# Kernel optimization log

Measured on AMD Instinct MI355X. Metric: run time of the kernel, lower is better.

## Reference

```python
import jax, jax.numpy as jnp
import numpy as np

TOKENS = 8192
IN_FEATURES = 4096
OUT_FEATURES = 4096
ALPHA = 2e-05
BETA = 8.0


def setup_inputs() -> dict:
    key = jax.random.key(0)
    kx, kw = jax.random.split(key)
    # int8 activations and weights, values in [-127, 127]
    x = jax.random.randint(kx, (TOKENS, IN_FEATURES), -127, 128, dtype=jnp.int32).astype(jnp.int8)
    weight = jax.random.randint(kw, (OUT_FEATURES, IN_FEATURES), -127, 128, dtype=jnp.int32).astype(jnp.int8)
    bias = jnp.zeros((OUT_FEATURES,), dtype=jnp.float32)
    a = jnp.float32(ALPHA)  # dequant scale: input_scale * weight_scale
    b = jnp.float32(BETA)   # requant scale: 1 / out_scale
    return {"x": x, "weight": weight, "bias": bias, "a": a, "b": b}


def reference(x, weight, bias, a, b):
    acc = jnp.matmul(x.astype(jnp.int32), weight.T.astype(jnp.int32))
    # fp32 epilogue: dequant scale + bias, exact GeLU, requant by beta
    y = a * acc.astype(jnp.float32) + bias[None, :]
    y = jax.nn.gelu(y, approximate=False)
    # quantize output to int8 (round to nearest even, saturate)
    q = jnp.clip(jnp.rint(y * b), -128.0, 127.0).astype(jnp.int8)
    return q
```

## Files before the change

### kernel.cpp

```cpp
#include <hip/hip_runtime.h>
#include <cstdint>
#include <cstddef>

#define TOKENS 8192
#define INF    4096
#define OUTF   4096

typedef int v4i __attribute__((ext_vector_type(4)));

__global__ __launch_bounds__(256) void pack_i8_kernel(
    const int* __restrict__ xi, const int* __restrict__ wi,
    uint8_t* __restrict__ x8, uint8_t* __restrict__ w8) {
  const int NX = (TOKENS * INF) / 4;
  const int NT = 2048 * 256;
  int tid = blockIdx.x * 256 + threadIdx.x;
#pragma unroll 1
  for (int g = 0; g < 6; ++g) {
    int c[4];
    int4 v[4];
#pragma unroll
    for (int j = 0; j < 4; ++j) {
      c[j] = (g * 4 + j) * NT + tid;
      const int4* src = (c[j] < NX) ? ((const int4*)xi + c[j])
                                    : ((const int4*)wi + (c[j] - NX));
      v[j] = *src;
    }
#pragma unroll
    for (int j = 0; j < 4; ++j) {
      unsigned* dst = (c[j] < NX) ? ((unsigned*)x8 + c[j])
                                  : ((unsigned*)w8 + (c[j] - NX));
      *dst = (v[j].x & 255) | ((v[j].y & 255) << 8) | ((v[j].z & 255) << 16) |
             (((unsigned)v[j].w) << 24);
    }
  }
}

__device__ __forceinline__ float gelu_exact(float y) {
  float x = y * 0.70710678118654752f;
  float s = fabsf(x);
  float t = __builtin_amdgcn_rcpf(fmaf(s, 0.3275911f, 1.0f));
  float p = t * fmaf(t, fmaf(t, fmaf(t, fmaf(t, 1.061405429f, -1.453152027f),
                                     1.421413741f), -0.284496736f),
                     0.254829592f);
  float e = __expf(-s * s);
  float er = fmaf(-p, e, 1.0f);
  er = copysignf(er, x);
  return 0.5f * y * (1.0f + er);
}

__device__ __forceinline__ void barrier_fenced() {
  asm volatile("" ::: "memory");
  __builtin_amdgcn_s_barrier();
  asm volatile("" ::: "memory");
}

__global__ __launch_bounds__(512, 2) void gemm_i8_gelu_q_kernel(
    const uint8_t* __restrict__ x8, const uint8_t* __restrict__ w8,
    const float* __restrict__ bias, const float* __restrict__ pa,
    const float* __restrict__ pb, int* __restrict__ out) {
  __shared__ char sm[131072];

  const int tid = threadIdx.x;
  const int l   = tid & 63;
  const int wv  = tid >> 6;
  const int wr  = wv >> 2;
  const int wc  = wv & 3;
  const int lr  = l & 15;
  const int lg  = l >> 4;

  int id = blockIdx.x;
  int wg = (id & 7) * 64 + (id >> 3);
  const int m0 = (wg >> 4) * 256;
  const int n0 = (wg & 15) * 256;

  const float av = pa[0];
  const float bv = pb[0];

  const int grow = (wv << 5) + (l >> 3);
  const int gch  = ((l & 7) ^ ((l >> 3) & 7)) << 4;
  const uint8_t* gA = x8 + (size_t)(m0 + grow) * INF + gch;
  const uint8_t* gB = w8 + (size_t)(n0 + grow) * INF + gch;
  const int dwv = wv * 4096;

  int aoff[8], boff[4], sb0, sb1;
#pragma unroll
  for (int m = 0; m < 8; ++m) aoff[m] = (wr * 128 + m * 16 + lr) * 128;
#pragma unroll
  for (int n = 0; n < 4; ++n) boff[n] = 32768 + (wc * 64 + n * 16 + lr) * 128;
  sb0 = ((0 + lg) ^ (l & 7)) << 4;
  sb1 = ((4 + lg) ^ (l & 7)) << 4;

  v4i acc[8][4];
#pragma unroll
  for (int m = 0; m < 8; ++m)
#pragma unroll
    for (int n = 0; n < 4; ++n) acc[m][n] = (v4i){0, 0, 0, 0};

#define GLL(gsrc, ldst)                                                       \
  __builtin_amdgcn_global_load_lds(                                           \
      (const __attribute__((address_space(1))) unsigned*)(gsrc),              \
      (__attribute__((address_space(3))) unsigned*)(ldst), 16, 0, 0);

#define GLA(T, J) GLL(gA + (size_t)(J) * 8 * INF + (size_t)(T) * 128,         \
                      sm + (((T) & 1) << 16) + dwv + (J) * 1024)
#define GLB(T, J) GLL(gB + (size_t)(J) * 8 * INF + (size_t)(T) * 128,         \
                      sm + (((T) & 1) << 16) + 32768 + dwv + (J) * 1024)

#define LD(off) (*(const v4i*)(sbr + (off)))
#define MM(ACC, AF, BF)                                                       \
  ACC = __builtin_amdgcn_mfma_i32_16x16x64_i8(AF, BF, ACC, 0, 0, 0)

#define PH_BAR                                                                \
  barrier_fenced();                                                           \
  asm volatile("s_waitcnt lgkmcnt(0)" ::: "memory");                          \
  __builtin_amdgcn_s_setprio(1);
#define PH_END __builtin_amdgcn_s_setprio(0);

#define ITER(DS)                                                              \
  {                                                                           \
    const char* sbr = sm + ((kt & 1) << 16);                                  \
    const int T = kt + 1;                                                     \
    v4i A0[4], A4[4], B0[2], B2[2];                                           \
                                           \
    A0[0] = LD(aoff[0] + sb0); A0[1] = LD(aoff[1] + sb0);                     \
    A0[2] = LD(aoff[2] + sb0); A0[3] = LD(aoff[3] + sb0);                     \
    B0[0] = LD(boff[0] + sb0); B0[1] = LD(boff[1] + sb0);                     \
    if (DS) { GLA(T, 0); GLA(T, 1); }                                         \
    PH_BAR                                               \
    MM(acc[0][0], A0[0], B0[0]); MM(acc[0][1], A0[0], B0[1]);                 \
    MM(acc[1][0], A0[1], B0[0]); MM(acc[1][1], A0[1], B0[1]);                 \
    MM(acc[2][0], A0[2], B0[0]); MM(acc[2][1], A0[2], B0[1]);                 \
    MM(acc[3][0], A0[3], B0[0]); MM(acc[3][1], A0[3], B0[1]);                 \
    PH_END                                                                    \
    A4[0] = LD(aoff[4] + sb0); A4[1] = LD(aoff[5] + sb0);                     \
    A4[2] = LD(aoff[6] + sb0); A4[3] = LD(aoff[7] + sb0);                     \
    if (DS) { GLA(T, 2); GLA(T, 3); }                                         \
    PH_BAR                                               \
    MM(acc[4][0], A4[0], B0[0]); MM(acc[4][1], A4[0], B0[1]);                 \
    MM(acc[5][0], A4[1], B0[0]); MM(acc[5][1], A4[1], B0[1]);                 \
    MM(acc[6][0], A4[2], B0[0]); MM(acc[6][1], A4[2], B0[1]);                 \
    MM(acc[7][0], A4[3], B0[0]); MM(acc[7][1], A4[3], B0[1]);                 \
    PH_END                                                                    \
    B2[0] = LD(boff[2] + sb0); B2[1] = LD(boff[3] + sb0);                     \
    if (DS) { GLB(T, 0); GLB(T, 1); }                                         \
    PH_BAR                                               \
    MM(acc[0][2], A0[0], B2[0]); MM(acc[0][3], A0[0], B2[1]);                 \
    MM(acc[1][2], A0[1], B2[0]); MM(acc[1][3], A0[1], B2[1]);                 \
    MM(acc[2][2], A0[2], B2[0]); MM(acc[2][3], A0[2], B2[1]);                 \
    MM(acc[3][2], A0[3], B2[0]); MM(acc[3][3], A0[3], B2[1]);                 \
    PH_END                                                                    \
    if (DS) { GLB(T, 2); GLB(T, 3); }                                         \
    PH_BAR                                               \
    MM(acc[4][2], A4[0], B2[0]); MM(acc[4][3], A4[0], B2[1]);                 \
    MM(acc[5][2], A4[1], B2[0]); MM(acc[5][3], A4[1], B2[1]);                 \
    MM(acc[6][2], A4[2], B2[0]); MM(acc[6][3], A4[2], B2[1]);                 \
    MM(acc[7][2], A4[3], B2[0]); MM(acc[7][3], A4[3], B2[1]);                 \
    PH_END                                                                    \
                              \
    A0[0] = LD(aoff[0] + sb1); A0[1] = LD(aoff[1] + sb1);                     \
    A0[2] = LD(aoff[2] + sb1); A0[3] = LD(aoff[3] + sb1);                     \
    B0[0] = LD(boff[0] + sb1); B0[1] = LD(boff[1] + sb1);                     \
    PH_BAR                                                            \
    MM(acc[0][0], A0[0], B0[0]); MM(acc[0][1], A0[0], B0[1]);                 \
    MM(acc[1][0], A0[1], B0[0]); MM(acc[1][1], A0[1], B0[1]);                 \
    MM(acc[2][0], A0[2], B0[0]); MM(acc[2][1], A0[2], B0[1]);                 \
    MM(acc[3][0], A0[3], B0[0]); MM(acc[3][1], A0[3], B0[1]);                 \
    PH_END                                                                    \
    A4[0] = LD(aoff[4] + sb1); A4[1] = LD(aoff[5] + sb1);                     \
    A4[2] = LD(aoff[6] + sb1); A4[3] = LD(aoff[7] + sb1);                     \
    PH_BAR                                                            \
    MM(acc[4][0], A4[0], B0[0]); MM(acc[4][1], A4[0], B0[1]);                 \
    MM(acc[5][0], A4[1], B0[0]); MM(acc[5][1], A4[1], B0[1]);                 \
    MM(acc[6][0], A4[2], B0[0]); MM(acc[6][1], A4[2], B0[1]);                 \
    MM(acc[7][0], A4[3], B0[0]); MM(acc[7][1], A4[3], B0[1]);                 \
    PH_END                                                                    \
    B2[0] = LD(boff[2] + sb1); B2[1] = LD(boff[3] + sb1);                     \
    PH_BAR                                                            \
    MM(acc[0][2], A0[0], B2[0]); MM(acc[0][3], A0[0], B2[1]);                 \
    MM(acc[1][2], A0[1], B2[0]); MM(acc[1][3], A0[1], B2[1]);                 \
    MM(acc[2][2], A0[2], B2[0]); MM(acc[2][3], A0[2], B2[1]);                 \
    MM(acc[3][2], A0[3], B2[0]); MM(acc[3][3], A0[3], B2[1]);                 \
    PH_END                                                                    \
    PH_BAR                                                            \
    MM(acc[4][2], A4[0], B2[0]); MM(acc[4][3], A4[0], B2[1]);                 \
    MM(acc[5][2], A4[1], B2[0]); MM(acc[5][3], A4[1], B2[1]);                 \
    MM(acc[6][2], A4[2], B2[0]); MM(acc[6][3], A4[2], B2[1]);                 \
    MM(acc[7][2], A4[3], B2[0]); MM(acc[7][3], A4[3], B2[1]);                 \
    PH_END                                                                    \
                  \
    if (DS) { asm volatile("s_waitcnt vmcnt(0)" ::: "memory"); }              \
    barrier_fenced();                                                         \
  }

  GLA(0, 0); GLA(0, 1); GLA(0, 2); GLA(0, 3);
  GLB(0, 0); GLB(0, 1); GLB(0, 2); GLB(0, 3);
  asm volatile("s_waitcnt vmcnt(0)" ::: "memory");
  barrier_fenced();

#pragma unroll 1
  for (int kt = 0; kt < 31; ++kt) ITER(1)
  {
    const int kt = 31;
    ITER(0)
  }

  float bvals[4];
#pragma unroll
  for (int n = 0; n < 4; ++n) bvals[n] = bias[n0 + wc * 64 + n * 16 + lr];

#pragma unroll
  for (int m = 0; m < 8; ++m) {
    int rowb = m0 + wr * 128 + m * 16 + lg * 4;
#pragma unroll
    for (int q = 0; q < 4; ++q) {
      size_t rb = (size_t)(rowb + q) * OUTF;
#pragma unroll
      for (int n = 0; n < 4; ++n) {
        float f = fmaf(av, (float)acc[m][n][q], bvals[n]);
        float g = gelu_exact(f);
        float r = __builtin_rintf(g * bv);
        r = fminf(fmaxf(r, -128.0f), 127.0f);
        out[rb + (size_t)(n0 + wc * 64 + n * 16 + lr)] = (int)r;
      }
    }
  }
#undef GLL
#undef GLA
#undef GLB
#undef LD
#undef MM
#undef PH_BAR
#undef PH_END
#undef ITER
}

extern "C" void kernel_launch(void* const* d_in, const int* in_sizes, int n_in,
                              void* d_out, int out_size, void* d_ws,
                              size_t ws_size, hipStream_t stream) {
  const int*   xi   = (const int*)d_in[0];
  const int*   wi   = (const int*)d_in[1];
  const float* bias = (const float*)d_in[2];
  const float* pa   = (const float*)d_in[3];
  const float* pb   = (const float*)d_in[4];
  int*         out  = (int*)d_out;

  uint8_t* x8 = (uint8_t*)d_ws;
  uint8_t* w8 = x8 + (size_t)TOKENS * INF;

  pack_i8_kernel<<<2048, 256, 0, stream>>>(xi, wi, x8, w8);

  dim3 grid((TOKENS / 256) * (OUTF / 256));
  gemm_i8_gelu_q_kernel<<<grid, 512, 0, stream>>>(x8, w8, bias, pa, pb, out);
}
```

Before: 400.2 us.

## Remove per-phase barriers from GEMM main loop and widen int8 pack stores

The main loop drops the eight per-phase workgroup barriers and explicit lgkmcnt waits, issues all eight global-to-LDS loads for the next tile at once, and then runs the MFMA blocks back to back, leaving only the single barrier at the end of each k-tile. This targets barrier stalls and scheduling overhead inside the inner loop, at the cost of less control over interleaving LDS reads, global loads and MFMAs, which now depends on the compiler. The pack kernel also changes so each thread packs 16 int32 values into one 16-byte store instead of four 4-byte stores.

```diff
diff --git a/kernel.cpp b/kernel.cpp
--- a/kernel.cpp
+++ b/kernel.cpp
@@ -11,27 +11,29 @@
 __global__ __launch_bounds__(256) void pack_i8_kernel(
     const int* __restrict__ xi, const int* __restrict__ wi,
     uint8_t* __restrict__ x8, uint8_t* __restrict__ w8) {
-  const int NX = (TOKENS * INF) / 4;
-  const int NT = 2048 * 256;
+  const int NXT = (TOKENS * INF) / 16;
+  const int NT  = 2048 * 256;
   int tid = blockIdx.x * 256 + threadIdx.x;
 #pragma unroll 1
   for (int g = 0; g < 6; ++g) {
-    int c[4];
-    int4 v[4];
-#pragma unroll
-    for (int j = 0; j < 4; ++j) {
-      c[j] = (g * 4 + j) * NT + tid;
-      const int4* src = (c[j] < NX) ? ((const int4*)xi + c[j])
-                                    : ((const int4*)wi + (c[j] - NX));
-      v[j] = *src;
+    int t = g * NT + tid;
+    const int4* s;
+    int4* d;
+    if (t < NXT) {
+      s = (const int4*)xi + 4 * (size_t)t;
+      d = (int4*)x8 + t;
+    } else {
+      int t2 = t - NXT;
+      s = (const int4*)wi + 4 * (size_t)t2;
+      d = (int4*)w8 + t2;
     }
-#pragma unroll
-    for (int j = 0; j < 4; ++j) {
-      unsigned* dst = (c[j] < NX) ? ((unsigned*)x8 + c[j])
-                                  : ((unsigned*)w8 + (c[j] - NX));
-      *dst = (v[j].x & 255) | ((v[j].y & 255) << 8) | ((v[j].z & 255) << 16) |
-             (((unsigned)v[j].w) << 24);
-    }
+    int4 v0 = s[0], v1 = s[1], v2 = s[2], v3 = s[3];
+    int4 p;
+    p.x = (v0.x & 255) | ((v0.y & 255) << 8) | ((v0.z & 255) << 16) | (v0.w << 24);
+    p.y = (v1.x & 255) | ((v1.y & 255) << 8) | ((v1.z & 255) << 16) | (v1.w << 24);
+    p.z = (v2.x & 255) | ((v2.y & 255) << 8) | ((v2.z & 255) << 16) | (v2.w << 24);
+    p.w = (v3.x & 255) | ((v3.y & 255) << 8) | ((v3.z & 255) << 16) | (v3.w << 24);
+    *d = p;
   }
 }
 
@@ -110,84 +112,57 @@
 #define MM(ACC, AF, BF)                                                       \
   ACC = __builtin_amdgcn_mfma_i32_16x16x64_i8(AF, BF, ACC, 0, 0, 0)
 
-#define PH_BAR                                                                \
-  barrier_fenced();                                                           \
-  asm volatile("s_waitcnt lgkmcnt(0)" ::: "memory");                          \
-  __builtin_amdgcn_s_setprio(1);
-#define PH_END __builtin_amdgcn_s_setprio(0);
+#define KSTEP                                                                 \
+  __builtin_amdgcn_s_setprio(1);                                              \
+  MM(acc[0][0], A0[0], B0[0]); MM(acc[0][1], A0[0], B0[1]);                   \
+  MM(acc[1][0], A0[1], B0[0]); MM(acc[1][1], A0[1], B0[1]);                   \
+  MM(acc[2][0], A0[2], B0[0]); MM(acc[2][1], A0[2], B0[1]);                   \
+  MM(acc[3][0], A0[3], B0[0]); MM(acc[3][1], A0[3], B0[1]);                   \
+  __builtin_amdgcn_s_setprio(0);                                              \
+  __builtin_amdgcn_s_setprio(1);                                              \
+  MM(acc[4][0], A4[0], B0[0]); MM(acc[4][1], A4[0], B0[1]);                   \
+  MM(acc[5][0], A4[1], B0[0]); MM(acc[5][1], A4[1], B0[1]);                   \
+  MM(acc[6][0], A4[2], B0[0]); MM(acc[6][1], A4[2], B0[1]);                   \
+  MM(acc[7][0], A4[3], B0[0]); MM(acc[7][1], A4[3], B0[1]);                   \
+  __builtin_amdgcn_s_setprio(0);                                              \
+  __builtin_amdgcn_s_setprio(1);                                              \
+  MM(acc[0][2], A0[0], B2[0]); MM(acc[0][3], A0[0], B2[1]);                   \
+  MM(acc[1][2], A0[1], B2[0]); MM(acc[1][3], A0[1], B2[1]);                   \
+  MM(acc[2][2], A0[2], B2[0]); MM(acc[2][3], A0[2], B2[1]);                   \
+  MM(acc[3][2], A0[3], B2[0]); MM(acc[3][3], A0[3], B2[1]);                   \
+  __builtin_amdgcn_s_setprio(0);                                              \
+  __builtin_amdgcn_s_setprio(1);                                              \
+  MM(acc[4][2], A4[0], B2[0]); MM(acc[4][3], A4[0], B2[1]);                   \
+  MM(acc[5][2], A4[1], B2[0]); MM(acc[5][3], A4[1], B2[1]);                   \
+  MM(acc[6][2], A4[2], B2[0]); MM(acc[6][3], A4[2], B2[1]);                   \
+  MM(acc[7][2], A4[3], B2[0]); MM(acc[7][3], A4[3], B2[1]);                   \
+  __builtin_amdgcn_s_setprio(0);
 
 #define ITER(DS)                                                              \
   {                                                                           \
     const char* sbr = sm + ((kt & 1) << 16);                                  \
     const int T = kt + 1;                                                     \
     v4i A0[4], A4[4], B0[2], B2[2];                                           \
-                                           \
+        \
     A0[0] = LD(aoff[0] + sb0); A0[1] = LD(aoff[1] + sb0);                     \
     A0[2] = LD(aoff[2] + sb0); A0[3] = LD(aoff[3] + sb0);                     \
     B0[0] = LD(boff[0] + sb0); B0[1] = LD(boff[1] + sb0);                     \
-    if (DS) { GLA(T, 0); GLA(T, 1); }                                         \
-    PH_BAR                                               \
-    MM(acc[0][0], A0[0], B0[0]); MM(acc[0][1], A0[0], B0[1]);                 \
-    MM(acc[1][0], A0[1], B0[0]); MM(acc[1][1], A0[1], B0[1]);                 \
-    MM(acc[2][0], A0[2], B0[0]); MM(acc[2][1], A0[2], B0[1]);                 \
-    MM(acc[3][0], A0[3], B0[0]); MM(acc[3][1], A0[3], B0[1]);                 \
-    PH_END                                                                    \
+    if (DS) {                                                                 \
+      GLA(T, 0); GLA(T, 1); GLA(T, 2); GLA(T, 3);                             \
+      GLB(T, 0); GLB(T, 1); GLB(T, 2); GLB(T, 3);                             \
+    }                                                                         \
     A4[0] = LD(aoff[4] + sb0); A4[1] = LD(aoff[5] + sb0);                     \
     A4[2] = LD(aoff[6] + sb0); A4[3] = LD(aoff[7] + sb0);                     \
-    if (DS) { GLA(T, 2); GLA(T, 3); }                                         \
-    PH_BAR                                               \
-    MM(acc[4][0], A4[0], B0[0]); MM(acc[4][1], A4[0], B0[1]);                 \
-    MM(acc[5][0], A4[1], B0[0]); MM(acc[5][1], A4[1], B0[1]);                 \
-    MM(acc[6][0], A4[2], B0[0]); MM(acc[6][1], A4[2], B0[1]);                 \
-    MM(acc[7][0], A4[3], B0[0]); MM(acc[7][1], A4[3], B0[1]);                 \
-    PH_END                                                                    \
     B2[0] = LD(boff[2] + sb0); B2[1] = LD(boff[3] + sb0);                     \
-    if (DS) { GLB(T, 0); GLB(T, 1); }                                         \
-    PH_BAR                                               \
-    MM(acc[0][2], A0[0], B2[0]); MM(acc[0][3], A0[0], B2[1]);                 \
-    MM(acc[1][2], A0[1], B2[0]); MM(acc[1][3], A0[1], B2[1]);                 \
-    MM(acc[2][2], A0[2], B2[0]); MM(acc[2][3], A0[2], B2[1]);                 \
-    MM(acc[3][2], A0[3], B2[0]); MM(acc[3][3], A0[3], B2[1]);                 \
-    PH_END                                                                    \
-    if (DS) { GLB(T, 2); GLB(T, 3); }                                         \
-    PH_BAR                                               \
-    MM(acc[4][2], A4[0], B2[0]); MM(acc[4][3], A4[0], B2[1]);                 \
-    MM(acc[5][2], A4[1], B2[0]); MM(acc[5][3], A4[1], B2[1]);                 \
-    MM(acc[6][2], A4[2], B2[0]); MM(acc[6][3], A4[2], B2[1]);                 \
-    MM(acc[7][2], A4[3], B2[0]); MM(acc[7][3], A4[3], B2[1]);                 \
-    PH_END                                                                    \
-                              \
+    KSTEP                                                                     \
     A0[0] = LD(aoff[0] + sb1); A0[1] = LD(aoff[1] + sb1);                     \
     A0[2] = LD(aoff[2] + sb1); A0[3] = LD(aoff[3] + sb1);                     \
     B0[0] = LD(boff[0] + sb1); B0[1] = LD(boff[1] + sb1);                     \
-    PH_BAR                                                            \
-    MM(acc[0][0], A0[0], B0[0]); MM(acc[0][1], A0[0], B0[1]);                 \
-    MM(acc[1][0], A0[1], B0[0]); MM(acc[1][1], A0[1], B0[1]);                 \
-    MM(acc[2][0], A0[2], B0[0]); MM(acc[2][1], A0[2], B0[1]);                 \
-    MM(acc[3][0], A0[3], B0[0]); MM(acc[3][1], A0[3], B0[1]);                 \
-    PH_END                                                                    \
     A4[0] = LD(aoff[4] + sb1); A4[1] = LD(aoff[5] + sb1);                     \
     A4[2] = LD(aoff[6] + sb1); A4[3] = LD(aoff[7] + sb1);                     \
-    PH_BAR                                                            \
-    MM(acc[4][0], A4[0], B0[0]); MM(acc[4][1], A4[0], B0[1]);                 \
-    MM(acc[5][0], A4[1], B0[0]); MM(acc[5][1], A4[1], B0[1]);                 \
-    MM(acc[6][0], A4[2], B0[0]); MM(acc[6][1], A4[2], B0[1]);                 \
-    MM(acc[7][0], A4[3], B0[0]); MM(acc[7][1], A4[3], B0[1]);                 \
-    PH_END                                                                    \
     B2[0] = LD(boff[2] + sb1); B2[1] = LD(boff[3] + sb1);                     \
-    PH_BAR                                                            \
-    MM(acc[0][2], A0[0], B2[0]); MM(acc[0][3], A0[0], B2[1]);                 \
-    MM(acc[1][2], A0[1], B2[0]); MM(acc[1][3], A0[1], B2[1]);                 \
-    MM(acc[2][2], A0[2], B2[0]); MM(acc[2][3], A0[2], B2[1]);                 \
-    MM(acc[3][2], A0[3], B2[0]); MM(acc[3][3], A0[3], B2[1]);                 \
-    PH_END                                                                    \
-    PH_BAR                                                            \
-    MM(acc[4][2], A4[0], B2[0]); MM(acc[4][3], A4[0], B2[1]);                 \
-    MM(acc[5][2], A4[1], B2[0]); MM(acc[5][3], A4[1], B2[1]);                 \
-    MM(acc[6][2], A4[2], B2[0]); MM(acc[6][3], A4[2], B2[1]);                 \
-    MM(acc[7][2], A4[3], B2[0]); MM(acc[7][3], A4[3], B2[1]);                 \
-    PH_END                                                                    \
-                  \
+    KSTEP                                                                     \
+          \
     if (DS) { asm volatile("s_waitcnt vmcnt(0)" ::: "memory"); }              \
     barrier_fenced();                                                         \
   }
@@ -229,8 +204,7 @@
 #undef GLB
 #undef LD
 #undef MM
-#undef PH_BAR
-#undef PH_END
+#undef KSTEP
 #undef ITER
 }
 
```

Result: faster. 388.0 us (-3.0%).
